# Kernel tuning notes

Hardware: AMD Instinct MI355X
Metric: run time of the kernel (lower is better)

Reference implementation:

```python
import jax, jax.numpy as jnp
import numpy as np

SEQ_LEN = 524288
TAGSET = 64
START = 62   # tag_to_ix['START_TAG']
STOP = 63    # tag_to_ix['STOP_TAG']
NEG = -10000.0


def setup_inputs() -> dict:
    key = jax.random.key(0)
    k1, k2 = jax.random.split(key)
    feats = jax.random.normal(k1, (SEQ_LEN, TAGSET), dtype=jnp.float32)
    # learned transition matrix; trans[next, prev], with START row / STOP col masked as in __init__
    trans = jax.random.normal(k2, (TAGSET, TAGSET), dtype=jnp.float32)
    trans = trans.at[START, :].set(NEG).at[:, STOP].set(NEG)
    return {"feats": feats, "trans": trans}


def reference(feats, trans):
    # Viterbi max-plus DP. forward_var fv[prev]; scores[next, prev] = fv[prev] + trans[next, prev]
    fv0 = jnp.full((TAGSET,), NEG, dtype=jnp.float32).at[START].set(0.0)

    def step(fv, feat):
        scores = fv[None, :] + trans            # [T_next, T_prev]
        bptr = jnp.argmax(scores, axis=1)        # best previous tag per next tag
        fv_new = jnp.max(scores, axis=1) + feat  # [T]
        return fv_new, bptr

    fv, bptrs = jax.lax.scan(step, fv0, feats)   # bptrs: [seq_len, T] int

    terminal = fv + trans[STOP]                  # transition to STOP
    best = jnp.argmax(terminal)
    path_score = terminal[best]

    # backtrack through backpointers (reverse scan), emitting tag at each step
    def back(tag, bp):
        return bp[tag], tag

    _, best_path = jax.lax.scan(back, best, bptrs, reverse=True)  # [seq_len] tags
    return path_score, best_path
```

## Files before the change

kernel.cpp:

```cpp
#include <hip/hip_runtime.h>
#include <hip/hip_bf16.h>

#define T_LEN 524288
#define NTAG 64
#define START_TAG 62
#define STOP_TAG 63
#define NEGV -10000.0f

#define KCH 2048
#define CL  256
#define WU  64

#define SG  64
#define NSG 32

typedef float v2f __attribute__((ext_vector_type(2)));

struct WaveLDS {
    __align__(16) float fv[2][NTAG];
    float trL[NTAG * 65];
};

static __device__ __forceinline__ float max3f(float a, float b, float c) {
    return fmaxf(fmaxf(a, b), c);
}
static __device__ __forceinline__ v2f mk2(float a, float b) {
    v2f r; r.x = a; r.y = b; return r;
}

template<int MODE>
__device__ __forceinline__ void wave_run(
    int t0, int nsteps, const float* __restrict__ feats,
    unsigned int* __restrict__ bpg, WaveLDS& L,
    const v2f* tr2, int lane)
{
    float fA[4], fB[4];
#pragma unroll
    for (int i = 0; i < 4; ++i)
        fA[i] = feats[(size_t)(t0 + i) * NTAG + lane];
    unsigned int acc = 0;
    const float* trrow = &L.trL[lane * 65];
#pragma unroll 1
    for (int tt = 0; tt < nsteps; tt += 4) {
        const bool hav = (tt + 4 < nsteps);
        if (hav) {
#pragma unroll
            for (int i = 0; i < 4; ++i)
                fB[i] = feats[(size_t)(t0 + tt + 4 + i) * NTAG + lane];
        }
#pragma unroll
        for (int s = 0; s < 4; ++s) {
            const int st = tt + s;
            const float* fvp = L.fv[st & 1];
            const float4* fq = (const float4*)fvp;
            float* fvn = L.fv[(st + 1) & 1];

            float gm[8];
#pragma unroll
            for (int g = 0; g < 8; ++g) {
                const float4 x0 = fq[2 * g + 0];
                const float4 x1 = fq[2 * g + 1];
                v2f a = mk2(x0.x, x0.y) + tr2[4 * g + 0];
                v2f b = mk2(x0.z, x0.w) + tr2[4 * g + 1];
                v2f c = mk2(x1.x, x1.y) + tr2[4 * g + 2];
                v2f d = mk2(x1.z, x1.w) + tr2[4 * g + 3];
                const float m1 = max3f(a.x, a.y, b.x);
                const float m2 = max3f(b.y, c.x, c.y);
                const float m3 = max3f(d.x, d.y, m1);
                gm[g] = fmaxf(m2, m3);
            }
            const float ga = max3f(gm[0], gm[1], gm[2]);
            const float gb = max3f(gm[3], gm[4], gm[5]);
            const float gc = max3f(gm[6], gm[7], ga);
            const float t  = fmaxf(gb, gc);
            fvn[lane] = t + fA[s];

            if (MODE == 1) {
                int g = 7;
                if (gm[6] == t) g = 6;
                if (gm[5] == t) g = 5;
                if (gm[4] == t) g = 4;
                if (gm[3] == t) g = 3;
                if (gm[2] == t) g = 2;
                if (gm[1] == t) g = 1;
                if (gm[0] == t) g = 0;
                const float* fg = fvp + (g << 3);
                const float4 y0 = *(const float4*)(fg);
                const float4 y1 = *(const float4*)(fg + 4);
                const float* tg = trrow + (g << 3);
                const float e0 = y0.x + tg[0], e1 = y0.y + tg[1];
                const float e2 = y0.z + tg[2], e3 = y0.w + tg[3];
                const float e4 = y1.x + tg[4], e5 = y1.y + tg[5];
                const float e6 = y1.z + tg[6], e7 = y1.w + tg[7];
                int j = 7;
                if (e6 == t) j = 6;
                if (e5 == t) j = 5;
                if (e4 == t) j = 4;
                if (e3 == t) j = 3;
                if (e2 == t) j = 2;
                if (e1 == t) j = 1;
                if (e0 == t) j = 0;
                const int idx = (g << 3) | j;
                acc |= (unsigned int)idx << (8 * s);
                if (s == 3) {
                    bpg[((size_t)(t0 + st - 3) >> 2) * NTAG + lane] = acc;
                    acc = 0;
                }
            }
        }
        if (hav) {
#pragma unroll
            for (int i = 0; i < 4; ++i) fA[i] = fB[i];
        }
    }
}

__device__ __forceinline__ void load_trans(const float* __restrict__ trans,
                                           int lane, v2f* tr2, float* trL)
{
    const float4* trow = (const float4*)(trans + (size_t)lane * NTAG);
#pragma unroll
    for (int j = 0; j < 16; ++j) {
        float4 v = trow[j];
        tr2[j * 2 + 0] = mk2(v.x, v.y);
        tr2[j * 2 + 1] = mk2(v.z, v.w);
        trL[lane * 65 + j * 4 + 0] = v.x;
        trL[lane * 65 + j * 4 + 1] = v.y;
        trL[lane * 65 + j * 4 + 2] = v.z;
        trL[lane * 65 + j * 4 + 3] = v.w;
    }
}

__global__ __launch_bounds__(64, 2) void pass1_kernel(
    const float* __restrict__ feats, const float* __restrict__ trans,
    unsigned int* __restrict__ bpg, float* __restrict__ ovl,
    float* __restrict__ bnd, unsigned char* __restrict__ maps)
{
    __shared__ WaveLDS L;
    const int lane = threadIdx.x;
    const int k = blockIdx.x;
    v2f tr2[32];
    load_trans(trans, lane, tr2, L.trL);

    if (k == 0) {
        L.fv[0][lane] = (lane == START_TAG) ? 0.0f : NEGV;
    } else {
        L.fv[0][lane] = 0.0f;
    }
    if (k > 0) {
        wave_run<0>(k * CL - WU, WU, feats, nullptr, L, tr2, lane);
        ovl[(size_t)k * NTAG + lane] = L.fv[0][lane];
    }
    wave_run<1>(k * CL, CL, feats, bpg, L, tr2, lane);
    bnd[(size_t)(k + 1) * NTAG + lane] = L.fv[0][lane];

    asm volatile("s_waitcnt vmcnt(0)" ::: "memory");
    int cur = lane;
    const size_t base = ((size_t)(k * CL) >> 2) * NTAG + lane;
#pragma unroll 4
    for (int t4 = CL / 4 - 1; t4 >= 0; --t4) {
        unsigned int b4 = bpg[base + (size_t)t4 * NTAG];
#pragma unroll
        for (int j = 3; j >= 0; --j) {
            unsigned int u = __shfl(b4, cur);
            cur = (u >> (8 * j)) & 255;
        }
    }
    maps[(size_t)k * NTAG + lane] = (unsigned char)cur;
}

__global__ __launch_bounds__(1024) void finalize_kernel(
    const float* __restrict__ bnd, const float* __restrict__ ovl,
    const float* __restrict__ trans, int* __restrict__ flags,
    float* __restrict__ dout, int* __restrict__ bestp)
{
    __shared__ float sc[16], se[16];
    __shared__ int sb[16];
    __shared__ float shift_sh;
    const int tid = threadIdx.x, w = tid >> 6, lane = tid & 63;
    float csum = 0.f, esum = 0.f;
    int bad = 0;
    for (int k = 1 + w; k < KCH; k += 16) {
        float d = bnd[(size_t)k * NTAG + lane] - ovl[(size_t)k * NTAG + lane];
        float d0 = __shfl(d, 0);
        float sp = fabsf(d - d0);
#pragma unroll
        for (int o = 1; o < 64; o <<= 1) sp = fmaxf(sp, __shfl_xor(sp, o));
        csum += d0; esum += sp;
        if (!(fabsf(d0) < 1.0e7f)) bad = 1;
    }
    if (lane == 0) { sc[w] = csum; se[w] = esum; sb[w] = bad; }
    __syncthreads();
    if (tid == 0) {
        float c = 0.f, e = 0.f; int b = 0;
        for (int i = 0; i < 16; ++i) { c += sc[i]; e += se[i]; b |= sb[i]; }
        if (!(e <= 1.0e4f)) b = 1;
        flags[0] = b;
        shift_sh = -c;
    }
    __syncthreads();
    if (tid < 64) {
        float shift = shift_sh;
        float v = (bnd[(size_t)KCH * NTAG + tid] - shift) + trans[STOP_TAG * NTAG + tid];
        int bi = tid;
#pragma unroll
        for (int o = 1; o < 64; o <<= 1) {
            float vo = __shfl_xor(v, o);
            int io = __shfl_xor(bi, o);
            if (vo > v || (vo == v && io < bi)) { v = vo; bi = io; }
        }
        if (tid == 0) { dout[0] = v; dout[T_LEN] = (float)bi; *bestp = bi; }
    }
}

__global__ __launch_bounds__(64) void fallback_kernel(
    const float* __restrict__ feats, const float* __restrict__ trans,
    int* __restrict__ flags, float* __restrict__ dout, int* __restrict__ bestp)
{
    __shared__ WaveLDS L;
    const int lane = threadIdx.x;
    if (flags[0] == 0) return;
    v2f tr2[32];
    load_trans(trans, lane, tr2, L.trL);
    L.fv[0][lane] = (lane == START_TAG) ? 0.0f : NEGV;
    wave_run<0>(0, T_LEN, feats, nullptr, L, tr2, lane);
    float v = L.fv[0][lane] + trans[STOP_TAG * NTAG + lane];
    int bi = lane;
#pragma unroll
    for (int o = 1; o < 64; o <<= 1) {
        float vo = __shfl_xor(v, o);
        int io = __shfl_xor(bi, o);
        if (vo > v || (vo == v && io < bi)) { v = vo; bi = io; }
    }
    if (lane == 0) { dout[0] = v; dout[T_LEN] = (float)bi; *bestp = bi; }
}

__global__ __launch_bounds__(64) void compose_kernel(
    const unsigned char* __restrict__ maps, unsigned char* __restrict__ smaps)
{
    const int lane = threadIdx.x, j = blockIdx.x;
    int cur = lane;
#pragma unroll 4
    for (int i = (j + 1) * SG - 1; i >= j * SG; --i) {
        int m = maps[(size_t)i * NTAG + lane];
        cur = __shfl(m, cur);
    }
    smaps[j * NTAG + lane] = (unsigned char)cur;
}

__global__ __launch_bounds__(64) void superchain_kernel(
    const unsigned char* __restrict__ smaps, const int* __restrict__ bestp,
    int* __restrict__ Esuper)
{
    const int lane = threadIdx.x;
    int e = *bestp;
#pragma unroll 1
    for (int j = NSG - 1; j >= 0; --j) {
        if (lane == 0) Esuper[j] = e;
        int m = smaps[j * NTAG + lane];
        e = __shfl(m, e);
    }
}

__global__ __launch_bounds__(64) void fill_kernel(
    const unsigned char* __restrict__ maps, const int* __restrict__ Esuper,
    unsigned char* __restrict__ Eblk)
{
    const int lane = threadIdx.x, j = blockIdx.x;
    int e = Esuper[j];
#pragma unroll 4
    for (int i = (j + 1) * SG - 1; i >= j * SG; --i) {
        if (lane == 0) Eblk[i] = (unsigned char)e;
        int m = maps[(size_t)i * NTAG + lane];
        e = __shfl(m, e);
    }
}

__global__ __launch_bounds__(64) void emit_kernel(
    const unsigned int* __restrict__ bpg, const unsigned char* __restrict__ Eblk,
    float* __restrict__ dout)
{
    const int lane = threadIdx.x, k = blockIdx.x;
    const int eblk = Eblk[k];
    int cur = lane;
    const int t0 = k * CL;
    const size_t base = ((size_t)t0 >> 2) * NTAG + lane;
#pragma unroll 4
    for (int t4 = CL / 4 - 1; t4 >= 0; --t4) {
        unsigned int b4 = bpg[base + (size_t)t4 * NTAG];
#pragma unroll
        for (int j = 3; j >= 0; --j) {
            unsigned int u = __shfl(b4, cur);
            cur = (u >> (8 * j)) & 255;
            const int t = t0 + t4 * 4 + j;
            if (t > 0 && lane == eblk) dout[t] = (float)cur;
        }
    }
}

__global__ void beacon_kernel(float* dout, float wsz) { dout[0] = wsz; }

extern "C" void kernel_launch(void* const* d_in, const int* in_sizes, int n_in,
                              void* d_out, int out_size, void* d_ws, size_t ws_size,
                              hipStream_t stream) {
    const float* feats = (const float*)d_in[0];
    const float* trans = (const float*)d_in[1];
    float* dout = (float*)d_out;
    char* ws = (char*)d_ws;

    size_t off = 0;
    auto alloc = [&](size_t bytes) -> void* {
        void* p = ws + off;
        off = (off + bytes + 255) & ~(size_t)255;
        return p;
    };
    unsigned int* bpg = (unsigned int*)alloc((size_t)(T_LEN / 4) * NTAG * 4);
    float* bnd    = (float*)alloc((size_t)(KCH + 1) * NTAG * sizeof(float));
    float* ovl    = (float*)alloc((size_t)KCH * NTAG * sizeof(float));
    int*   flags  = (int*)alloc(256);
    unsigned char* maps  = (unsigned char*)alloc((size_t)KCH * NTAG);
    unsigned char* smaps = (unsigned char*)alloc((size_t)NSG * NTAG);
    int*   Esuper = (int*)alloc(NSG * sizeof(int));
    unsigned char* Eblk  = (unsigned char*)alloc(KCH);
    int*   bestp  = (int*)alloc(sizeof(int));
    const size_t NEED = off;

    if (ws_size < NEED) {
        beacon_kernel<<<1, 1, 0, stream>>>(dout, (float)ws_size);
        return;
    }

    pass1_kernel<<<KCH, 64, 0, stream>>>(feats, trans, bpg, ovl, bnd, maps);
    finalize_kernel<<<1, 1024, 0, stream>>>(bnd, ovl, trans, flags, dout, bestp);
    fallback_kernel<<<1, 64, 0, stream>>>(feats, trans, flags, dout, bestp);
    compose_kernel<<<NSG, 64, 0, stream>>>(maps, smaps);
    superchain_kernel<<<1, 64, 0, stream>>>(smaps, bestp, Esuper);
    fill_kernel<<<NSG, 64, 0, stream>>>(maps, Esuper, Eblk);
    emit_kernel<<<KCH, 64, 0, stream>>>(bpg, Eblk, dout);
}
```

Measured before the change: 468.6 us.

## Halve chunk length, pack four waves per block, move transitions to shared LDS

Doubles the number of sequence chunks (4096 chunks of 128 steps) so the serial per-chunk DP chain is shorter, and packs four chunk-waves into one 256-thread block that shares one LDS copy of the transition matrix. The per-lane register copy of transitions is dropped in favour of LDS reads, which frees registers for higher occupancy but adds LDS traffic in the inner max loop. The boundary-consistency reduction is split into a 64-block partial kernel plus a final one-wave kernel to handle the larger chunk count. The 64-step warmup is now a larger fraction of each shorter chunk, and more chunks feed the compose and emit stages.

```diff
diff --git a/kernel.cpp b/kernel.cpp
--- a/kernel.cpp
+++ b/kernel.cpp
@@ -7,39 +7,35 @@
 #define STOP_TAG 63
 #define NEGV -10000.0f
 
-#define KCH 2048
-#define CL  256
+#define KCH 4096
+#define CL  128
 #define WU  64
+#define WPB 4
 
 #define SG  64
-#define NSG 32
-
-typedef float v2f __attribute__((ext_vector_type(2)));
-
-struct WaveLDS {
-    __align__(16) float fv[2][NTAG];
+#define NSG (KCH / SG)
+
+struct BlockLDS {
     float trL[NTAG * 65];
+    __align__(16) float fv[WPB][2][NTAG];
 };
 
 static __device__ __forceinline__ float max3f(float a, float b, float c) {
     return fmaxf(fmaxf(a, b), c);
-}
-static __device__ __forceinline__ v2f mk2(float a, float b) {
-    v2f r; r.x = a; r.y = b; return r;
 }
 
 template<int MODE>
 __device__ __forceinline__ void wave_run(
     int t0, int nsteps, const float* __restrict__ feats,
-    unsigned int* __restrict__ bpg, WaveLDS& L,
-    const v2f* tr2, int lane)
-{
+    unsigned int* __restrict__ bpg, float (*fv)[NTAG],
+    const float* __restrict__ trL, int lane)
+{
+    const float* trrow = &trL[lane * 65];
     float fA[4], fB[4];
 #pragma unroll
     for (int i = 0; i < 4; ++i)
         fA[i] = feats[(size_t)(t0 + i) * NTAG + lane];
     unsigned int acc = 0;
-    const float* trrow = &L.trL[lane * 65];
 #pragma unroll 1
     for (int tt = 0; tt < nsteps; tt += 4) {
         const bool hav = (tt + 4 < nsteps);
@@ -51,22 +47,23 @@
 #pragma unroll
         for (int s = 0; s < 4; ++s) {
             const int st = tt + s;
-            const float* fvp = L.fv[st & 1];
+            const float* fvp = fv[st & 1];
             const float4* fq = (const float4*)fvp;
-            float* fvn = L.fv[(st + 1) & 1];
+            float* fvn = fv[(st + 1) & 1];
 
             float gm[8];
 #pragma unroll
             for (int g = 0; g < 8; ++g) {
                 const float4 x0 = fq[2 * g + 0];
                 const float4 x1 = fq[2 * g + 1];
-                v2f a = mk2(x0.x, x0.y) + tr2[4 * g + 0];
-                v2f b = mk2(x0.z, x0.w) + tr2[4 * g + 1];
-                v2f c = mk2(x1.x, x1.y) + tr2[4 * g + 2];
-                v2f d = mk2(x1.z, x1.w) + tr2[4 * g + 3];
-                const float m1 = max3f(a.x, a.y, b.x);
-                const float m2 = max3f(b.y, c.x, c.y);
-                const float m3 = max3f(d.x, d.y, m1);
+                const float* tg = trrow + g * 8;
+                const float c0 = x0.x + tg[0], c1 = x0.y + tg[1];
+                const float c2 = x0.z + tg[2], c3 = x0.w + tg[3];
+                const float c4 = x1.x + tg[4], c5 = x1.y + tg[5];
+                const float c6 = x1.z + tg[6], c7 = x1.w + tg[7];
+                const float m1 = max3f(c0, c1, c2);
+                const float m2 = max3f(c3, c4, c5);
+                const float m3 = max3f(c6, c7, m1);
                 gm[g] = fmaxf(m2, m3);
             }
             const float ga = max3f(gm[0], gm[1], gm[2]);
@@ -84,9 +81,9 @@
                 if (gm[2] == t) g = 2;
                 if (gm[1] == t) g = 1;
                 if (gm[0] == t) g = 0;
-                const float* fg = fvp + (g << 3);
-                const float4 y0 = *(const float4*)(fg);
-                const float4 y1 = *(const float4*)(fg + 4);
+                const float4* yq = (const float4*)(fvp + (g << 3));
+                const float4 y0 = yq[0];
+                const float4 y1 = yq[1];
                 const float* tg = trrow + (g << 3);
                 const float e0 = y0.x + tg[0], e1 = y0.y + tg[1];
                 const float e2 = y0.z + tg[2], e3 = y0.w + tg[3];
@@ -115,44 +112,42 @@
     }
 }
 
-__device__ __forceinline__ void load_trans(const float* __restrict__ trans,
-                                           int lane, v2f* tr2, float* trL)
+__device__ __forceinline__ void load_trans_lds(const float* __restrict__ trans,
+                                               int lane, float* trL)
 {
     const float4* trow = (const float4*)(trans + (size_t)lane * NTAG);
+    float* dst = trL + lane * 65;
 #pragma unroll
     for (int j = 0; j < 16; ++j) {
         float4 v = trow[j];
-        tr2[j * 2 + 0] = mk2(v.x, v.y);
-        tr2[j * 2 + 1] = mk2(v.z, v.w);
-        trL[lane * 65 + j * 4 + 0] = v.x;
-        trL[lane * 65 + j * 4 + 1] = v.y;
-        trL[lane * 65 + j * 4 + 2] = v.z;
-        trL[lane * 65 + j * 4 + 3] = v.w;
-    }
-}
-
-__global__ __launch_bounds__(64, 2) void pass1_kernel(
+        dst[j * 4 + 0] = v.x; dst[j * 4 + 1] = v.y;
+        dst[j * 4 + 2] = v.z; dst[j * 4 + 3] = v.w;
+    }
+}
+
+__global__ __launch_bounds__(256, 4) void pass1_kernel(
     const float* __restrict__ feats, const float* __restrict__ trans,
     unsigned int* __restrict__ bpg, float* __restrict__ ovl,
     float* __restrict__ bnd, unsigned char* __restrict__ maps)
 {
-    __shared__ WaveLDS L;
-    const int lane = threadIdx.x;
-    const int k = blockIdx.x;
-    v2f tr2[32];
-    load_trans(trans, lane, tr2, L.trL);
-
+    __shared__ BlockLDS L;
+    const int lane = threadIdx.x & 63;
+    const int w = threadIdx.x >> 6;
+    const int k = blockIdx.x * WPB + w;
+    load_trans_lds(trans, lane, L.trL);
+
+    float (*fv)[NTAG] = L.fv[w];
     if (k == 0) {
-        L.fv[0][lane] = (lane == START_TAG) ? 0.0f : NEGV;
+        fv[0][lane] = (lane == START_TAG) ? 0.0f : NEGV;
     } else {
-        L.fv[0][lane] = 0.0f;
+        fv[0][lane] = 0.0f;
     }
     if (k > 0) {
-        wave_run<0>(k * CL - WU, WU, feats, nullptr, L, tr2, lane);
-        ovl[(size_t)k * NTAG + lane] = L.fv[0][lane];
-    }
-    wave_run<1>(k * CL, CL, feats, bpg, L, tr2, lane);
-    bnd[(size_t)(k + 1) * NTAG + lane] = L.fv[0][lane];
+        wave_run<0>(k * CL - WU, WU, feats, nullptr, fv, L.trL, lane);
+        ovl[(size_t)k * NTAG + lane] = fv[0][lane];
+    }
+    wave_run<1>(k * CL, CL, feats, bpg, fv, L.trL, lane);
+    bnd[(size_t)(k + 1) * NTAG + lane] = fv[0][lane];
 
     asm volatile("s_waitcnt vmcnt(0)" ::: "memory");
     int cur = lane;
@@ -169,18 +164,17 @@
     maps[(size_t)k * NTAG + lane] = (unsigned char)cur;
 }
 
-__global__ __launch_bounds__(1024) void finalize_kernel(
+__global__ __launch_bounds__(1024) void finalize_part_kernel(
     const float* __restrict__ bnd, const float* __restrict__ ovl,
-    const float* __restrict__ trans, int* __restrict__ flags,
-    float* __restrict__ dout, int* __restrict__ bestp)
+    float* __restrict__ pc, float* __restrict__ pe, int* __restrict__ pb)
 {
     __shared__ float sc[16], se[16];
     __shared__ int sb[16];
-    __shared__ float shift_sh;
     const int tid = threadIdx.x, w = tid >> 6, lane = tid & 63;
+    const int gw = blockIdx.x * 16 + w;
     float csum = 0.f, esum = 0.f;
     int bad = 0;
-    for (int k = 1 + w; k < KCH; k += 16) {
+    for (int k = 1 + gw; k < KCH; k += 1024) {
         float d = bnd[(size_t)k * NTAG + lane] - ovl[(size_t)k * NTAG + lane];
         float d0 = __shfl(d, 0);
         float sp = fabsf(d - d0);
@@ -194,37 +188,51 @@
     if (tid == 0) {
         float c = 0.f, e = 0.f; int b = 0;
         for (int i = 0; i < 16; ++i) { c += sc[i]; e += se[i]; b |= sb[i]; }
-        if (!(e <= 1.0e4f)) b = 1;
-        flags[0] = b;
-        shift_sh = -c;
-    }
-    __syncthreads();
-    if (tid < 64) {
-        float shift = shift_sh;
-        float v = (bnd[(size_t)KCH * NTAG + tid] - shift) + trans[STOP_TAG * NTAG + tid];
-        int bi = tid;
-#pragma unroll
-        for (int o = 1; o < 64; o <<= 1) {
-            float vo = __shfl_xor(v, o);
-            int io = __shfl_xor(bi, o);
-            if (vo > v || (vo == v && io < bi)) { v = vo; bi = io; }
-        }
-        if (tid == 0) { dout[0] = v; dout[T_LEN] = (float)bi; *bestp = bi; }
-    }
+        pc[blockIdx.x] = c; pe[blockIdx.x] = e; pb[blockIdx.x] = b;
+    }
+}
+
+__global__ __launch_bounds__(64) void finalize_final_kernel(
+    const float* __restrict__ bnd, const float* __restrict__ trans,
+    const float* __restrict__ pc, const float* __restrict__ pe,
+    const int* __restrict__ pb, int* __restrict__ flags,
+    float* __restrict__ dout, int* __restrict__ bestp)
+{
+    const int tid = threadIdx.x;
+    float c = pc[tid], e = pe[tid];
+    int b = pb[tid];
+#pragma unroll
+    for (int o = 1; o < 64; o <<= 1) {
+        c += __shfl_xor(c, o);
+        e += __shfl_xor(e, o);
+        b |= __shfl_xor(b, o);
+    }
+    if (!(e <= 1.0e4f)) b = 1;
+    if (tid == 0) flags[0] = b;
+    const float shift = -c;
+    float v = (bnd[(size_t)KCH * NTAG + tid] - shift) + trans[STOP_TAG * NTAG + tid];
+    int bi = tid;
+#pragma unroll
+    for (int o = 1; o < 64; o <<= 1) {
+        float vo = __shfl_xor(v, o);
+        int io = __shfl_xor(bi, o);
+        if (vo > v || (vo == v && io < bi)) { v = vo; bi = io; }
+    }
+    if (tid == 0) { dout[0] = v; dout[T_LEN] = (float)bi; *bestp = bi; }
 }
 
 __global__ __launch_bounds__(64) void fallback_kernel(
     const float* __restrict__ feats, const float* __restrict__ trans,
     int* __restrict__ flags, float* __restrict__ dout, int* __restrict__ bestp)
 {
-    __shared__ WaveLDS L;
+    __shared__ float trL[NTAG * 65];
+    __shared__ __align__(16) float fv[2][NTAG];
     const int lane = threadIdx.x;
     if (flags[0] == 0) return;
-    v2f tr2[32];
-    load_trans(trans, lane, tr2, L.trL);
-    L.fv[0][lane] = (lane == START_TAG) ? 0.0f : NEGV;
-    wave_run<0>(0, T_LEN, feats, nullptr, L, tr2, lane);
-    float v = L.fv[0][lane] + trans[STOP_TAG * NTAG + lane];
+    load_trans_lds(trans, lane, trL);
+    fv[0][lane] = (lane == START_TAG) ? 0.0f : NEGV;
+    wave_run<0>(0, T_LEN, feats, nullptr, fv, trL, lane);
+    float v = fv[0][lane] + trans[STOP_TAG * NTAG + lane];
     int bi = lane;
 #pragma unroll
     for (int o = 1; o < 64; o <<= 1) {
@@ -323,6 +331,9 @@
     int*   Esuper = (int*)alloc(NSG * sizeof(int));
     unsigned char* Eblk  = (unsigned char*)alloc(KCH);
     int*   bestp  = (int*)alloc(sizeof(int));
+    float* pc     = (float*)alloc(64 * sizeof(float));
+    float* pe     = (float*)alloc(64 * sizeof(float));
+    int*   pb     = (int*)alloc(64 * sizeof(int));
     const size_t NEED = off;
 
     if (ws_size < NEED) {
@@ -330,8 +341,9 @@
         return;
     }
 
-    pass1_kernel<<<KCH, 64, 0, stream>>>(feats, trans, bpg, ovl, bnd, maps);
-    finalize_kernel<<<1, 1024, 0, stream>>>(bnd, ovl, trans, flags, dout, bestp);
+    pass1_kernel<<<KCH / WPB, 256, 0, stream>>>(feats, trans, bpg, ovl, bnd, maps);
+    finalize_part_kernel<<<64, 1024, 0, stream>>>(bnd, ovl, pc, pe, pb);
+    finalize_final_kernel<<<1, 64, 0, stream>>>(bnd, trans, pc, pe, pb, flags, dout, bestp);
     fallback_kernel<<<1, 64, 0, stream>>>(feats, trans, flags, dout, bestp);
     compose_kernel<<<NSG, 64, 0, stream>>>(maps, smaps);
     superchain_kernel<<<1, 64, 0, stream>>>(smaps, bestp, Esuper);
```

Measured after the change: 432.8 us. 1.08x faster.
